# Kernel tuning notes

Measured on AMD Instinct MI355X. Metric: run time of the kernel, lower is better.

Reference implementation:

```python
import jax, jax.numpy as jnp
import numpy as np


def setup_inputs() -> dict:
    key = jax.random.key(0)
    kA, kB = jax.random.split(key)
    B, H, W, C = 1, 80, 80, 256  # NHWC backbone features; B must be 1 for the TF broadcast in the divide to be valid
    feature_A = jax.random.normal(kA, (B, H, W, C), dtype=jnp.float32)
    feature_B = jax.random.normal(kB, (B, H, W, C), dtype=jnp.float32)
    return {"feature_A": feature_A, "feature_B": feature_B}


def reference(feature_A, feature_B):
    # corr[b,i,j,k,l] = mean_c A[b,i,j,c] * B[b,k,l,c]
    # Expressed as a batched matmul instead of materializing the (H,W,H,W,C) intermediate.
    C = feature_A.shape[-1]
    corr = jnp.einsum('bijc,bklc->bijkl', feature_A, feature_B) / C  # [B,H,W,H,W]
    # penalty[b,i,j] = sqrt(sum_{k,l} corr^2)
    penalty = jnp.sqrt(jnp.sum(corr * corr, axis=(-1, -2)))  # [B,H,W]
    # Faithful to tf.math.divide: trailing-dim broadcasting of [B,H,W] against [B,H,W,H,W]
    # (valid because B == 1; penalty aligns to the (j,k,l) trailing axes exactly as in TF).
    return corr / penalty
```

## Files before the change

kernel.cpp:

```cpp
#include <hip/hip_runtime.h>

typedef __attribute__((ext_vector_type(8))) short bf16x8;
typedef __attribute__((ext_vector_type(4))) float f32x4;

#define M_TOT 6400
#define C_TOT 256
#define BM 128
#define BN 128
#define BK 32
#define NTILE 50
#define ONM 50
#define ONN 25

#define VMCNT0 asm volatile("s_waitcnt vmcnt(0)" ::: "memory")
#define VMCNT4 asm volatile("s_waitcnt vmcnt(4)" ::: "memory")
#define VMCNT6 asm volatile("s_waitcnt vmcnt(6)" ::: "memory")
#define SBAR   __builtin_amdgcn_s_barrier()

__device__ __forceinline__ short f2bf(float f) {
    unsigned u = __float_as_uint(f);
    u = (u + 0x7fffu + ((u >> 16) & 1u)) >> 16;
    return (short)u;
}
__device__ __forceinline__ float bf2f(short s) {
    return __uint_as_float(((unsigned)(unsigned short)s) << 16);
}

__device__ __forceinline__ void gload16(const short* g, short* l) {
    __builtin_amdgcn_global_load_lds(
        (const __attribute__((address_space(1))) void*)g,
        (__attribute__((address_space(3))) void*)l, 16, 0, 0);
}


__global__ __launch_bounds__(256) void prep(const float* __restrict__ A,
                                            const float* __restrict__ Bm,
                                            short* __restrict__ Ab,
                                            short* __restrict__ Bb,
                                            short* __restrict__ Bt,
                                            float* __restrict__ P)
{
    __shared__ __align__(16) short Lb[64][72];
    const int bid = blockIdx.x;
    const int t   = threadIdx.x;

    if (bid < 400) {
        const int n0 = (bid % 100) * 64;
        const int c0 = (bid / 100) * 64;
        const int r  = t >> 2;
        const int cb = (t & 3) * 16;

        const float4* src = reinterpret_cast<const float4*>(
            Bm + (size_t)(n0 + r) * C_TOT + c0 + cb);
        const float4 v0 = src[0], v1 = src[1], v2 = src[2], v3 = src[3];
        bf16x8 w0, w1;
        w0[0]=f2bf(v0.x); w0[1]=f2bf(v0.y); w0[2]=f2bf(v0.z); w0[3]=f2bf(v0.w);
        w0[4]=f2bf(v1.x); w0[5]=f2bf(v1.y); w0[6]=f2bf(v1.z); w0[7]=f2bf(v1.w);
        w1[0]=f2bf(v2.x); w1[1]=f2bf(v2.y); w1[2]=f2bf(v2.z); w1[3]=f2bf(v2.w);
        w1[4]=f2bf(v3.x); w1[5]=f2bf(v3.y); w1[6]=f2bf(v3.z); w1[7]=f2bf(v3.w);
        *reinterpret_cast<bf16x8*>(&Lb[r][cb])     = w0;
        *reinterpret_cast<bf16x8*>(&Lb[r][cb + 8]) = w1;
        short* brow = Bb + (size_t)(n0 + r) * C_TOT + c0 + cb;
        *reinterpret_cast<bf16x8*>(brow)     = w0;
        *reinterpret_cast<bf16x8*>(brow + 8) = w1;
        __syncthreads();

        #pragma unroll
        for (int p = 0; p < 2; ++p) {
            const int q = t + p * 256;
            const int c = q >> 3;
            const int h = q & 7;
            bf16x8 w;
            #pragma unroll
            for (int j = 0; j < 8; ++j) w[j] = Lb[h * 8 + j][c];
            *reinterpret_cast<bf16x8*>(&Bt[(size_t)(c0 + c) * M_TOT + n0 + h * 8]) = w;
        }
    } else {
        const int aid = bid - 400;
        if (aid == 0)
            for (int j = t; j < M_TOT; j += 256) P[j] = 0.0f;
        const int base = aid * 2048;
        #pragma unroll
        for (int it = 0; it < 8; ++it) {
            const int i = base + it * 256 + t;
            const float4 v0 = reinterpret_cast<const float4*>(A + (size_t)i * 8)[0];
            const float4 v1 = reinterpret_cast<const float4*>(A + (size_t)i * 8)[1];
            bf16x8 w;
            w[0]=f2bf(v0.x); w[1]=f2bf(v0.y); w[2]=f2bf(v0.z); w[3]=f2bf(v0.w);
            w[4]=f2bf(v1.x); w[5]=f2bf(v1.y); w[6]=f2bf(v1.z); w[7]=f2bf(v1.w);
            *reinterpret_cast<bf16x8*>(Ab + (size_t)i * 8) = w;
        }
    }
}

__global__ __launch_bounds__(256) void convert_ab(const float* __restrict__ A,
                                                  const float* __restrict__ Bm,
                                                  short* __restrict__ Ab,
                                                  short* __restrict__ Bb)
{
    const int n8 = M_TOT * C_TOT / 8;
    for (int i = blockIdx.x * blockDim.x + threadIdx.x; i < 2 * n8;
         i += gridDim.x * blockDim.x) {
        const float* s = (i < n8) ? (A + (size_t)i * 8) : (Bm + (size_t)(i - n8) * 8);
        short* d       = (i < n8) ? (Ab + (size_t)i * 8) : (Bb + (size_t)(i - n8) * 8);
        const float4 v0 = reinterpret_cast<const float4*>(s)[0];
        const float4 v1 = reinterpret_cast<const float4*>(s)[1];
        bf16x8 w;
        w[0]=f2bf(v0.x); w[1]=f2bf(v0.y); w[2]=f2bf(v0.z); w[3]=f2bf(v0.w);
        w[4]=f2bf(v1.x); w[5]=f2bf(v1.y); w[6]=f2bf(v1.z); w[7]=f2bf(v1.w);
        *reinterpret_cast<bf16x8*>(d) = w;
    }
}


__device__ __forceinline__ void stage_tiles_g(const short* __restrict__ A,
                                              const short* __restrict__ B,
                                              int m0, int n0, int k0,
                                              int lda, int ldb,
                                              short* As, short* Bs,
                                              int wave, int lane)
{
    #pragma unroll
    for (int t = 0; t < 2; ++t) {
        const int c  = (wave * 2 + t) * 64 + lane;
        const int r  = c >> 2;
        const int g  = c & 3;
        const int sg = g ^ ((r >> 1) & 3);
        gload16(A + (size_t)(m0 + r) * lda + k0 + sg * 8, As + (wave * 2 + t) * 512);
        gload16(B + (size_t)(n0 + r) * ldb + k0 + sg * 8, Bs + (wave * 2 + t) * 512);
    }
}

template<int KSTEPS>
__device__ __forceinline__ void gemm_tile_g(const short* __restrict__ A,
                                            const short* __restrict__ B,
                                            int m0, int n0, int kbase,
                                            int lda, int ldb, int tid,
                                            short (*Sm)[2][4096],
                                            f32x4 acc[4][4])
{
    const int lane = tid & 63;
    const int wave = tid >> 6;
    const int rl   = lane & 15;
    const int g_rd = lane >> 4;
    const int wr   = wave >> 1;
    const int wc   = wave & 1;

    stage_tiles_g(A, B, m0, n0, kbase, lda, ldb, &Sm[0][0][0], &Sm[0][1][0], wave, lane);
    if (KSTEPS > 1)
        stage_tiles_g(A, B, m0, n0, kbase + BK, lda, ldb,
                      &Sm[1][0][0], &Sm[1][1][0], wave, lane);
    if (KSTEPS > 1) { VMCNT4; } else { VMCNT0; }
    SBAR;

    #pragma unroll
    for (int kt = 0; kt < KSTEPS; ++kt) {
        const int cur = kt % 3;
        if (kt + 2 < KSTEPS)
            stage_tiles_g(A, B, m0, n0, kbase + (kt + 2) * BK, lda, ldb,
                          &Sm[(kt + 2) % 3][0][0], &Sm[(kt + 2) % 3][1][0], wave, lane);

        bf16x8 af[4], bfr[4];
        #pragma unroll
        for (int mi = 0; mi < 4; ++mi) {
            const int r  = wr * 64 + mi * 16 + rl;
            const int sg = g_rd ^ ((r >> 1) & 3);
            af[mi] = *reinterpret_cast<const bf16x8*>(&Sm[cur][0][r * BK + sg * 8]);
        }
        #pragma unroll
        for (int ni = 0; ni < 4; ++ni) {
            const int r  = wc * 64 + ni * 16 + rl;
            const int sg = g_rd ^ ((r >> 1) & 3);
            bfr[ni] = *reinterpret_cast<const bf16x8*>(&Sm[cur][1][r * BK + sg * 8]);
        }
        __builtin_amdgcn_s_setprio(1);
        #pragma unroll
        for (int mi = 0; mi < 4; ++mi)
            #pragma unroll
            for (int ni = 0; ni < 4; ++ni)
                acc[mi][ni] = __builtin_amdgcn_mfma_f32_16x16x32_bf16(
                    af[mi], bfr[ni], acc[mi][ni], 0, 0, 0);
        __builtin_amdgcn_s_setprio(0);

        if (kt + 1 < KSTEPS) {
            if (kt + 2 < KSTEPS) { VMCNT4; } else { VMCNT0; }
            SBAR;
        }
    }
}


template<int STEPS>
__global__ __launch_bounds__(256) void gemm_G(const short* __restrict__ Bt,
                                              float* __restrict__ Gp)
{
    __shared__ __align__(16) short Sm[3][2][4096];
    const int tid = threadIdx.x;
    const int m0 = blockIdx.y * BM, n0 = blockIdx.x * BN;
    const int z  = blockIdx.z;
    f32x4 acc[4][4] = {};
    gemm_tile_g<STEPS>(Bt, Bt, m0, n0, z * (STEPS * BK),
                       M_TOT, M_TOT, tid, Sm, acc);

    float* dst = Gp + (size_t)z * (C_TOT * C_TOT);
    const int lane = tid & 63, rl = lane & 15;
    const int wave = tid >> 6, wr = wave >> 1, wc = wave & 1;
    #pragma unroll
    for (int mi = 0; mi < 4; ++mi)
        #pragma unroll
        for (int i = 0; i < 4; ++i) {
            const int m = m0 + wr * 64 + mi * 16 + (lane >> 4) * 4 + i;
            #pragma unroll
            for (int ni = 0; ni < 4; ++ni)
                dst[m * C_TOT + n0 + wc * 64 + ni * 16 + rl] = acc[mi][ni][i];
        }
}

__global__ __launch_bounds__(256) void g_reduce(const float* __restrict__ Gp,
                                                short* __restrict__ Gb,
                                                int nchunks)
{
    const int i4 = blockIdx.x * 256 + threadIdx.x;
    float4 s = make_float4(0.f, 0.f, 0.f, 0.f);
    for (int z = 0; z < nchunks; ++z) {
        const float4 v = reinterpret_cast<const float4*>(
            Gp + (size_t)z * (C_TOT * C_TOT))[i4];
        s.x += v.x; s.y += v.y; s.z += v.z; s.w += v.w;
    }
    short4 o;
    o.x = f2bf(s.x); o.y = f2bf(s.y); o.z = f2bf(s.z); o.w = f2bf(s.w);
    reinterpret_cast<short4*>(Gb)[i4] = o;
}

__global__ __launch_bounds__(256) void penalty_q(const short* __restrict__ Ab,
                                                 const short* __restrict__ Gb,
                                                 float* __restrict__ P)
{
    __shared__ __align__(16) short Sm[3][2][4096];
    const int tid = threadIdx.x;
    const int m0 = blockIdx.x * BM;
    const int ci = blockIdx.y & 1, cj = blockIdx.y >> 1;
    const int lane = tid & 63, rl = lane & 15;
    const int wave = tid >> 6, wr = wave >> 1, wc = wave & 1;

    f32x4 acc[4][4] = {};
    gemm_tile_g<4>(Ab, Gb + (size_t)(cj * BM) * C_TOT, m0, 0, ci * BM,
                   C_TOT, C_TOT, tid, Sm, acc);

    #pragma unroll
    for (int mi = 0; mi < 4; ++mi)
        #pragma unroll
        for (int i = 0; i < 4; ++i) {
            const int m = m0 + wr * 64 + mi * 16 + (lane >> 4) * 4 + i;
            float s = 0.0f;
            #pragma unroll
            for (int ni = 0; ni < 4; ++ni) {
                const int cp = cj * BM + wc * 64 + ni * 16 + rl;
                s += acc[mi][ni][i] * bf2f(Ab[(size_t)m * C_TOT + cp]);
            }
            s += __shfl_xor(s, 1);
            s += __shfl_xor(s, 2);
            s += __shfl_xor(s, 4);
            s += __shfl_xor(s, 8);
            if (rl == 0) atomicAdd(&P[m], s);
        }
}


#define OBUF 12288
#define OB_B 4096

__device__ __forceinline__ void stage_tiles_o(const short* __restrict__ A,
                                              const short* __restrict__ B,
                                              int m0, int n0, int k0,
                                              short* buf, int wave, int lane)
{
    #pragma unroll
    for (int t = 0; t < 2; ++t) {
        const int c  = (wave * 2 + t) * 64 + lane;
        const int r  = c >> 2;
        const int g  = c & 3;
        const int sg = g ^ ((r >> 1) & 3);
        gload16(A + (size_t)(m0 + r) * C_TOT + k0 + sg * 8, buf + (wave * 2 + t) * 512);
    }
    #pragma unroll
    for (int t = 0; t < 4; ++t) {
        const int c  = (wave * 4 + t) * 64 + lane;
        const int r  = c >> 2;
        const int g  = c & 3;
        const int sg = g ^ ((r >> 1) & 3);
        gload16(B + (size_t)(n0 + r) * C_TOT + k0 + sg * 8,
                buf + OB_B + (wave * 4 + t) * 512);
    }
}

__global__ __launch_bounds__(256, 2) void gemm_out(const short* __restrict__ Ab,
                                                   const short* __restrict__ Bb,
                                                   const float* __restrict__ P,
                                                   float* __restrict__ out)
{
    __shared__ __align__(16) short Sm[3][OBUF];
    const int tid = threadIdx.x;
    const int lane = tid & 63, rl = lane & 15;
    const int g_rd = lane >> 4;
    const int wave = tid >> 6, wr = wave >> 1, wc = wave & 1;

    const int nwg = ONM * ONN, q = nwg >> 3, r = nwg & 7;
    const int orig = blockIdx.x;
    const int xcd = orig & 7, idx = orig >> 3;
    const int wg = (xcd < r ? xcd * (q + 1) : r * (q + 1) + (xcd - r) * q) + idx;
    const int m0 = (wg / ONN) * 128;
    const int n0 = (wg % ONN) * 256;

    f32x4 acc[4][8] = {};

    stage_tiles_o(Ab, Bb, m0, n0, 0,  &Sm[0][0], wave, lane);
    stage_tiles_o(Ab, Bb, m0, n0, BK, &Sm[1][0], wave, lane);
    VMCNT6; SBAR;

    #pragma unroll
    for (int kt = 0; kt < 8; ++kt) {
        const int cur = kt % 3;
        if (kt + 2 < 8)
            stage_tiles_o(Ab, Bb, m0, n0, (kt + 2) * BK, &Sm[(kt + 2) % 3][0], wave, lane);

        bf16x8 af[4], bfr[8];
        #pragma unroll
        for (int mi = 0; mi < 4; ++mi) {
            const int rr = wr * 64 + mi * 16 + rl;
            const int sg = g_rd ^ ((rr >> 1) & 3);
            af[mi] = *reinterpret_cast<const bf16x8*>(&Sm[cur][rr * BK + sg * 8]);
        }
        #pragma unroll
        for (int ni = 0; ni < 8; ++ni) {
            const int rr = wc * 128 + ni * 16 + rl;
            const int sg = g_rd ^ ((rr >> 1) & 3);
            bfr[ni] = *reinterpret_cast<const bf16x8*>(&Sm[cur][OB_B + rr * BK + sg * 8]);
        }
        __builtin_amdgcn_s_setprio(1);
        #pragma unroll
        for (int mi = 0; mi < 4; ++mi)
            #pragma unroll
            for (int ni = 0; ni < 8; ++ni)
                acc[mi][ni] = __builtin_amdgcn_mfma_f32_16x16x32_bf16(
                    af[mi], bfr[ni], acc[mi][ni], 0, 0, 0);
        __builtin_amdgcn_s_setprio(0);

        if (kt + 1 < 8) {
            if (kt + 2 < 8) { VMCNT6; } else { VMCNT0; }
            SBAR;
        }
    }

    float rs[8];
    #pragma unroll
    for (int ni = 0; ni < 8; ++ni)
        rs[ni] = rsqrtf(P[n0 + wc * 128 + ni * 16 + rl]);

    SBAR;

    float* Es = reinterpret_cast<float*>(Sm) + wave * 2112;
    #pragma unroll
    for (int mi = 0; mi < 4; ++mi) {
        #pragma unroll
        for (int ni = 0; ni < 8; ++ni)
            #pragma unroll
            for (int i = 0; i < 4; ++i)
                Es[((lane >> 4) * 4 + i) * 132 + ni * 16 + rl] = acc[mi][ni][i] * rs[ni];
        #pragma unroll
        for (int it = 0; it < 8; ++it) {
            const int f   = it * 64 + lane;
            const int row = f >> 5;
            const int c4  = f & 31;
            const float4 v = *reinterpret_cast<const float4*>(&Es[row * 132 + c4 * 4]);
            const int m = m0 + wr * 64 + mi * 16 + row;
            *reinterpret_cast<float4*>(
                &out[(size_t)m * M_TOT + n0 + wc * 128 + c4 * 4]) = v;
        }
    }
}


__global__ __launch_bounds__(256) void gemm_penalty(const short* __restrict__ Ab,
                                                    const short* __restrict__ Bb,
                                                    float* __restrict__ P)
{
    __shared__ __align__(16) short Sm[3][2][4096];
    const int tid = threadIdx.x;
    const int m0 = blockIdx.y * BM, n0 = blockIdx.x * BN;
    f32x4 acc[4][4] = {};
    gemm_tile_g<8>(Ab, Bb, m0, n0, 0, C_TOT, C_TOT, tid, Sm, acc);

    const int lane = tid & 63, rl = lane & 15;
    const int wave = tid >> 6, wr = wave >> 1;
    #pragma unroll
    for (int mi = 0; mi < 4; ++mi) {
        #pragma unroll
        for (int i = 0; i < 4; ++i) {
            const int m = m0 + wr * 64 + mi * 16 + (lane >> 4) * 4 + i;
            float s = 0.0f;
            #pragma unroll
            for (int ni = 0; ni < 4; ++ni) {
                const float v = acc[mi][ni][i];
                s += v * v;
            }
            s += __shfl_xor(s, 1);
            s += __shfl_xor(s, 2);
            s += __shfl_xor(s, 4);
            s += __shfl_xor(s, 8);
            if (rl == 0) atomicAdd(&P[m], s);
        }
    }
}

__global__ __launch_bounds__(256) void gemm_out_plain(const short* __restrict__ Ab,
                                                      const short* __restrict__ Bb,
                                                      const float* __restrict__ P,
                                                      float* __restrict__ out)
{
    __shared__ __align__(16) short Sm[3][2][4096];
    const int tid = threadIdx.x;
    const int lane = tid & 63, rl = lane & 15;
    const int wave = tid >> 6, wr = wave >> 1, wc = wave & 1;
    const int m0 = blockIdx.y * BM, n0 = blockIdx.x * BN;

    f32x4 acc[4][4] = {};
    gemm_tile_g<8>(Ab, Bb, m0, n0, 0, C_TOT, C_TOT, tid, Sm, acc);

    float rs[4];
    #pragma unroll
    for (int ni = 0; ni < 4; ++ni)
        rs[ni] = rsqrtf(P[n0 + wc * 64 + ni * 16 + rl]);

    SBAR;

    float* Es = reinterpret_cast<float*>(Sm) + wave * 1088;
    #pragma unroll
    for (int mi = 0; mi < 4; ++mi) {
        #pragma unroll
        for (int ni = 0; ni < 4; ++ni)
            #pragma unroll
            for (int i = 0; i < 4; ++i)
                Es[((lane >> 4) * 4 + i) * 68 + ni * 16 + rl] = acc[mi][ni][i] * rs[ni];
        #pragma unroll
        for (int it = 0; it < 4; ++it) {
            const int f   = it * 64 + lane;
            const int row = f >> 4;
            const int c4  = f & 15;
            const float4 v = *reinterpret_cast<const float4*>(&Es[row * 68 + c4 * 4]);
            const int m = m0 + wr * 64 + mi * 16 + row;
            *reinterpret_cast<float4*>(&out[(size_t)m * M_TOT + n0 + wc * 64 + c4 * 4]) = v;
        }
    }
}


__global__ __launch_bounds__(256) void corr_gemm(const float* __restrict__ A,
                                                 const float* __restrict__ Bm,
                                                 float* __restrict__ out,
                                                 float* __restrict__ penalty)
{
    __shared__ short As[BM * BK];
    __shared__ short Bs[BN * BK];

    const int tid  = threadIdx.x;
    const int lane = tid & 63;
    const int wave = tid >> 6;
    const int wr   = wave >> 1;
    const int wc   = wave & 1;
    const int m0   = blockIdx.y * BM;
    const int n0   = blockIdx.x * BN;
    const int g_rd = lane >> 4;
    const int rl   = lane & 15;

    f32x4 acc[4][4] = {};

    for (int k0 = 0; k0 < C_TOT; k0 += BK) {
        #pragma unroll
        for (int half = 0; half < 2; ++half) {
            const int cc = tid + half * 256;
            const int r  = cc >> 2;
            const int g  = cc & 3;
            const int sg = g ^ ((r >> 1) & 3);

            const float4* pa = reinterpret_cast<const float4*>(
                A + (size_t)(m0 + r) * C_TOT + k0 + g * 8);
            float4 a0 = pa[0], a1 = pa[1];
            bf16x8 wa;
            wa[0]=f2bf(a0.x); wa[1]=f2bf(a0.y); wa[2]=f2bf(a0.z); wa[3]=f2bf(a0.w);
            wa[4]=f2bf(a1.x); wa[5]=f2bf(a1.y); wa[6]=f2bf(a1.z); wa[7]=f2bf(a1.w);
            *reinterpret_cast<bf16x8*>(&As[r * BK + sg * 8]) = wa;

            const float4* pb = reinterpret_cast<const float4*>(
                Bm + (size_t)(n0 + r) * C_TOT + k0 + g * 8);
            float4 b0 = pb[0], b1 = pb[1];
            bf16x8 wb;
            wb[0]=f2bf(b0.x); wb[1]=f2bf(b0.y); wb[2]=f2bf(b0.z); wb[3]=f2bf(b0.w);
            wb[4]=f2bf(b1.x); wb[5]=f2bf(b1.y); wb[6]=f2bf(b1.z); wb[7]=f2bf(b1.w);
            *reinterpret_cast<bf16x8*>(&Bs[r * BK + sg * 8]) = wb;
        }
        __syncthreads();

        bf16x8 af[4], bfr[4];
        #pragma unroll
        for (int mi = 0; mi < 4; ++mi) {
            const int r  = wr * 64 + mi * 16 + rl;
            const int sg = g_rd ^ ((r >> 1) & 3);
            af[mi] = *reinterpret_cast<const bf16x8*>(&As[r * BK + sg * 8]);
        }
        #pragma unroll
        for (int ni = 0; ni < 4; ++ni) {
            const int r  = wc * 64 + ni * 16 + rl;
            const int sg = g_rd ^ ((r >> 1) & 3);
            bfr[ni] = *reinterpret_cast<const bf16x8*>(&Bs[r * BK + sg * 8]);
        }
        #pragma unroll
        for (int mi = 0; mi < 4; ++mi)
            #pragma unroll
            for (int ni = 0; ni < 4; ++ni)
                acc[mi][ni] = __builtin_amdgcn_mfma_f32_16x16x32_bf16(
                    af[mi], bfr[ni], acc[mi][ni], 0, 0, 0);
        __syncthreads();
    }

    const float inv_c = 1.0f / (float)C_TOT;
    #pragma unroll
    for (int mi = 0; mi < 4; ++mi) {
        #pragma unroll
        for (int i = 0; i < 4; ++i) {
            const int m = m0 + wr * 64 + mi * 16 + (lane >> 4) * 4 + i;
            float s = 0.0f;
            #pragma unroll
            for (int ni = 0; ni < 4; ++ni) {
                const float v = acc[mi][ni][i] * inv_c;
                out[(size_t)m * M_TOT + n0 + wc * 64 + ni * 16 + rl] = v;
                s += v * v;
            }
            s += __shfl_xor(s, 1);
            s += __shfl_xor(s, 2);
            s += __shfl_xor(s, 4);
            s += __shfl_xor(s, 8);
            if (rl == 0) atomicAdd(&penalty[m], s);
        }
    }
}

__global__ __launch_bounds__(256) void scale_k(float* __restrict__ out,
                                               const float* __restrict__ penalty)
{
    const unsigned cols4 = M_TOT / 4;
    const unsigned total = (unsigned)M_TOT * cols4;
    float4* o4 = reinterpret_cast<float4*>(out);
    const float4* p4 = reinterpret_cast<const float4*>(penalty);
    for (unsigned idx = blockIdx.x * blockDim.x + threadIdx.x; idx < total;
         idx += gridDim.x * blockDim.x) {
        const unsigned n4 = idx % cols4;
        const float4 p = p4[n4];
        float4 v = o4[idx];
        v.x *= rsqrtf(p.x);
        v.y *= rsqrtf(p.y);
        v.z *= rsqrtf(p.z);
        v.w *= rsqrtf(p.w);
        o4[idx] = v;
    }
}


extern "C" void kernel_launch(void* const* d_in, const int* in_sizes, int n_in,
                              void* d_out, int out_size, void* d_ws, size_t ws_size,
                              hipStream_t stream) {
    const float* A = (const float*)d_in[0];
    const float* B = (const float*)d_in[1];
    float* out     = (float*)d_out;

    const size_t mat_sh = (size_t)M_TOT * C_TOT;
    const size_t sz_ab  = mat_sh * sizeof(short);
    const size_t sz_gb  = (size_t)C_TOT * C_TOT * sizeof(short);
    const size_t sz_p   = (size_t)M_TOT * sizeof(float);
    const size_t sz_gq  = (size_t)C_TOT * C_TOT * sizeof(float);
    const size_t base_need = 3 * sz_ab + sz_gb + sz_p;
    const size_t need_f40  = base_need + 40 * sz_gq;
    const size_t need_f20  = base_need + 20 * sz_gq;
    const size_t need_mid  = 2 * sz_ab + sz_p;

    dim3 grid2(NTILE, NTILE);

    if (ws_size >= need_f20) {
        short* Ab = (short*)d_ws;
        short* Bb = Ab + mat_sh;
        short* Bt = Bb + mat_sh;
        short* Gb = Bt + mat_sh;
        float* P  = (float*)((char*)d_ws + 3 * sz_ab + sz_gb);
        float* Gp = (float*)((char*)d_ws + 3 * sz_ab + sz_gb + sz_p);

        prep<<<500, 256, 0, stream>>>(A, B, Ab, Bb, Bt, P);
        if (ws_size >= need_f40) {
            gemm_G<5><<<dim3(2, 2, 40), 256, 0, stream>>>(Bt, Gp);
            g_reduce<<<64, 256, 0, stream>>>(Gp, Gb, 40);
        } else {
            gemm_G<10><<<dim3(2, 2, 20), 256, 0, stream>>>(Bt, Gp);
            g_reduce<<<64, 256, 0, stream>>>(Gp, Gb, 20);
        }
        penalty_q<<<dim3(NTILE, 4), 256, 0, stream>>>(Ab, Gb, P);
        gemm_out<<<ONM * ONN, 256, 0, stream>>>(Ab, Bb, P, out);
    } else if (ws_size >= need_mid) {
        short* Ab = (short*)d_ws;
        short* Bb = Ab + mat_sh;
        float* P  = (float*)(Bb + mat_sh);

        hipMemsetAsync(P, 0, sz_p, stream);
        convert_ab<<<1600, 256, 0, stream>>>(A, B, Ab, Bb);
        gemm_penalty<<<grid2, dim3(256), 0, stream>>>(Ab, Bb, P);
        gemm_out_plain<<<grid2, dim3(256), 0, stream>>>(Ab, Bb, P, out);
    } else {
        float* penalty = (float*)d_ws;
        hipMemsetAsync(penalty, 0, sz_p, stream);
        corr_gemm<<<grid2, dim3(256), 0, stream>>>(A, B, out, penalty);
        scale_k<<<2048, 256, 0, stream>>>(out, penalty);
    }
}
```

Before: 84.01 us.

## Fuse prep, Gram GEMM, reduce and penalty into one cooperative kernel

```diff
diff --git a/kernel.cpp b/kernel.cpp
--- a/kernel.cpp
+++ b/kernel.cpp
@@ -1,4 +1,7 @@
 #include <hip/hip_runtime.h>
+#include <hip/hip_cooperative_groups.h>
+
+namespace cg = cooperative_groups;
 
 typedef __attribute__((ext_vector_type(8))) short bf16x8;
 typedef __attribute__((ext_vector_type(4))) float f32x4;
@@ -11,6 +14,7 @@
 #define NTILE 50
 #define ONM 50
 #define ONN 25
+#define GZ  50
 
 #define VMCNT0 asm volatile("s_waitcnt vmcnt(0)" ::: "memory")
 #define VMCNT4 asm volatile("s_waitcnt vmcnt(4)" ::: "memory")
@@ -30,6 +34,219 @@
     __builtin_amdgcn_global_load_lds(
         (const __attribute__((address_space(1))) void*)g,
         (__attribute__((address_space(3))) void*)l, 16, 0, 0);
+}
+
+
+__device__ __forceinline__ void stage_tiles_g(const short* __restrict__ A,
+                                              const short* __restrict__ B,
+                                              int m0, int n0, int k0,
+                                              int lda, int ldb,
+                                              short* As, short* Bs,
+                                              int wave, int lane)
+{
+    #pragma unroll
+    for (int t = 0; t < 2; ++t) {
+        const int c  = (wave * 2 + t) * 64 + lane;
+        const int r  = c >> 2;
+        const int g  = c & 3;
+        const int sg = g ^ ((r >> 1) & 3);
+        gload16(A + (size_t)(m0 + r) * lda + k0 + sg * 8, As + (wave * 2 + t) * 512);
+        gload16(B + (size_t)(n0 + r) * ldb + k0 + sg * 8, Bs + (wave * 2 + t) * 512);
+    }
+}
+
+template<int KSTEPS>
+__device__ __forceinline__ void gemm_tile_g(const short* __restrict__ A,
+                                            const short* __restrict__ B,
+                                            int m0, int n0, int kbase,
+                                            int lda, int ldb, int tid,
+                                            short (*Sm)[2][4096],
+                                            f32x4 acc[4][4])
+{
+    const int lane = tid & 63;
+    const int wave = tid >> 6;
+    const int rl   = lane & 15;
+    const int g_rd = lane >> 4;
+    const int wr   = wave >> 1;
+    const int wc   = wave & 1;
+
+    stage_tiles_g(A, B, m0, n0, kbase, lda, ldb, &Sm[0][0][0], &Sm[0][1][0], wave, lane);
+    if (KSTEPS > 1)
+        stage_tiles_g(A, B, m0, n0, kbase + BK, lda, ldb,
+                      &Sm[1][0][0], &Sm[1][1][0], wave, lane);
+    if (KSTEPS > 1) { VMCNT4; } else { VMCNT0; }
+    SBAR;
+
+    #pragma unroll
+    for (int kt = 0; kt < KSTEPS; ++kt) {
+        const int cur = kt % 3;
+        if (kt + 2 < KSTEPS)
+            stage_tiles_g(A, B, m0, n0, kbase + (kt + 2) * BK, lda, ldb,
+                          &Sm[(kt + 2) % 3][0][0], &Sm[(kt + 2) % 3][1][0], wave, lane);
+
+        bf16x8 af[4], bfr[4];
+        #pragma unroll
+        for (int mi = 0; mi < 4; ++mi) {
+            const int r  = wr * 64 + mi * 16 + rl;
+            const int sg = g_rd ^ ((r >> 1) & 3);
+            af[mi] = *reinterpret_cast<const bf16x8*>(&Sm[cur][0][r * BK + sg * 8]);
+        }
+        #pragma unroll
+        for (int ni = 0; ni < 4; ++ni) {
+            const int r  = wc * 64 + ni * 16 + rl;
+            const int sg = g_rd ^ ((r >> 1) & 3);
+            bfr[ni] = *reinterpret_cast<const bf16x8*>(&Sm[cur][1][r * BK + sg * 8]);
+        }
+        __builtin_amdgcn_s_setprio(1);
+        #pragma unroll
+        for (int mi = 0; mi < 4; ++mi)
+            #pragma unroll
+            for (int ni = 0; ni < 4; ++ni)
+                acc[mi][ni] = __builtin_amdgcn_mfma_f32_16x16x32_bf16(
+                    af[mi], bfr[ni], acc[mi][ni], 0, 0, 0);
+        __builtin_amdgcn_s_setprio(0);
+
+        if (kt + 1 < KSTEPS) {
+            if (kt + 2 < KSTEPS) { VMCNT4; } else { VMCNT0; }
+            SBAR;
+        }
+    }
+}
+
+
+__global__ __launch_bounds__(256) void fused_pre(const float* __restrict__ A,
+                                                 const float* __restrict__ Bm,
+                                                 short* __restrict__ Ab,
+                                                 short* __restrict__ Bb,
+                                                 short* __restrict__ Bt,
+                                                 short* __restrict__ Gb,
+                                                 float* __restrict__ P,
+                                                 float* __restrict__ Gp)
+{
+    cg::grid_group grid = cg::this_grid();
+    __shared__ __align__(16) short Sm[3][2][4096];
+    const int bid = blockIdx.x;
+    const int t   = threadIdx.x;
+
+    for (int u = bid; u < 500; u += 256) {
+        if (u < 400) {
+            short (*Lb)[72] = reinterpret_cast<short(*)[72]>(&Sm[0][0][0]);
+            const int n0 = (u % 100) * 64;
+            const int c0 = (u / 100) * 64;
+            const int r  = t >> 2;
+            const int cb = (t & 3) * 16;
+
+            const float4* src = reinterpret_cast<const float4*>(
+                Bm + (size_t)(n0 + r) * C_TOT + c0 + cb);
+            const float4 v0 = src[0], v1 = src[1], v2 = src[2], v3 = src[3];
+            bf16x8 w0, w1;
+            w0[0]=f2bf(v0.x); w0[1]=f2bf(v0.y); w0[2]=f2bf(v0.z); w0[3]=f2bf(v0.w);
+            w0[4]=f2bf(v1.x); w0[5]=f2bf(v1.y); w0[6]=f2bf(v1.z); w0[7]=f2bf(v1.w);
+            w1[0]=f2bf(v2.x); w1[1]=f2bf(v2.y); w1[2]=f2bf(v2.z); w1[3]=f2bf(v2.w);
+            w1[4]=f2bf(v3.x); w1[5]=f2bf(v3.y); w1[6]=f2bf(v3.z); w1[7]=f2bf(v3.w);
+            *reinterpret_cast<bf16x8*>(&Lb[r][cb])     = w0;
+            *reinterpret_cast<bf16x8*>(&Lb[r][cb + 8]) = w1;
+            short* brow = Bb + (size_t)(n0 + r) * C_TOT + c0 + cb;
+            *reinterpret_cast<bf16x8*>(brow)     = w0;
+            *reinterpret_cast<bf16x8*>(brow + 8) = w1;
+            __syncthreads();
+
+            #pragma unroll
+            for (int p = 0; p < 2; ++p) {
+                const int q = t + p * 256;
+                const int c = q >> 3;
+                const int h = q & 7;
+                bf16x8 w;
+                #pragma unroll
+                for (int j = 0; j < 8; ++j) w[j] = Lb[h * 8 + j][c];
+                *reinterpret_cast<bf16x8*>(&Bt[(size_t)(c0 + c) * M_TOT + n0 + h * 8]) = w;
+            }
+            __syncthreads();
+        } else {
+            const int aid = u - 400;
+            if (aid == 0)
+                for (int j = t; j < M_TOT; j += 256) P[j] = 0.0f;
+            const int base = aid * 2048;
+            #pragma unroll
+            for (int it = 0; it < 8; ++it) {
+                const int i = base + it * 256 + t;
+                const float4 v0 = reinterpret_cast<const float4*>(A + (size_t)i * 8)[0];
+                const float4 v1 = reinterpret_cast<const float4*>(A + (size_t)i * 8)[1];
+                bf16x8 w;
+                w[0]=f2bf(v0.x); w[1]=f2bf(v0.y); w[2]=f2bf(v0.z); w[3]=f2bf(v0.w);
+                w[4]=f2bf(v1.x); w[5]=f2bf(v1.y); w[6]=f2bf(v1.z); w[7]=f2bf(v1.w);
+                *reinterpret_cast<bf16x8*>(Ab + (size_t)i * 8) = w;
+            }
+        }
+    }
+    grid.sync();
+
+    if (bid < 4 * GZ) {
+        const int z  = bid >> 2;
+        const int qd = bid & 3;
+        const int m0 = (qd & 1) * BM, n0 = (qd >> 1) * BN;
+        f32x4 acc[4][4] = {};
+        gemm_tile_g<4>(Bt, Bt, m0, n0, z * 128, M_TOT, M_TOT, t, Sm, acc);
+
+        float* dst = Gp + (size_t)z * (C_TOT * C_TOT);
+        const int lane = t & 63, rl = lane & 15;
+        const int wave = t >> 6, wr = wave >> 1, wc = wave & 1;
+        #pragma unroll
+        for (int mi = 0; mi < 4; ++mi)
+            #pragma unroll
+            for (int i = 0; i < 4; ++i) {
+                const int m = m0 + wr * 64 + mi * 16 + (lane >> 4) * 4 + i;
+                #pragma unroll
+                for (int ni = 0; ni < 4; ++ni)
+                    dst[m * C_TOT + n0 + wc * 64 + ni * 16 + rl] = acc[mi][ni][i];
+            }
+    }
+    grid.sync();
+
+    if (bid < 64) {
+        const int i4 = bid * 256 + t;
+        float4 s = make_float4(0.f, 0.f, 0.f, 0.f);
+        for (int z = 0; z < GZ; ++z) {
+            const float4 v = reinterpret_cast<const float4*>(
+                Gp + (size_t)z * (C_TOT * C_TOT))[i4];
+            s.x += v.x; s.y += v.y; s.z += v.z; s.w += v.w;
+        }
+        short4 o;
+        o.x = f2bf(s.x); o.y = f2bf(s.y); o.z = f2bf(s.z); o.w = f2bf(s.w);
+        reinterpret_cast<short4*>(Gb)[i4] = o;
+    }
+    grid.sync();
+
+    if (bid < 200) {
+        const int mt = bid % 50;
+        const int qd = bid / 50;
+        const int ci = qd & 1, cj = qd >> 1;
+        const int m0 = mt * BM;
+        const int lane = t & 63, rl = lane & 15;
+        const int wave = t >> 6, wr = wave >> 1, wc = wave & 1;
+
+        f32x4 acc[4][4] = {};
+        gemm_tile_g<4>(Ab, Gb + (size_t)(cj * BM) * C_TOT, m0, 0, ci * BM,
+                       C_TOT, C_TOT, t, Sm, acc);
+
+        #pragma unroll
+        for (int mi = 0; mi < 4; ++mi)
+            #pragma unroll
+            for (int i = 0; i < 4; ++i) {
+                const int m = m0 + wr * 64 + mi * 16 + (lane >> 4) * 4 + i;
+                float s = 0.0f;
+                #pragma unroll
+                for (int ni = 0; ni < 4; ++ni) {
+                    const int cp = cj * BM + wc * 64 + ni * 16 + rl;
+                    s += acc[mi][ni][i] * bf2f(Ab[(size_t)m * C_TOT + cp]);
+                }
+                s += __shfl_xor(s, 1);
+                s += __shfl_xor(s, 2);
+                s += __shfl_xor(s, 4);
+                s += __shfl_xor(s, 8);
+                if (rl == 0) atomicAdd(&P[m], s);
+            }
+    }
 }
 
 
@@ -93,6 +310,197 @@
     }
 }
 
+template<int STEPS>
+__global__ __launch_bounds__(256) void gemm_G(const short* __restrict__ Bt,
+                                              float* __restrict__ Gp)
+{
+    __shared__ __align__(16) short Sm[3][2][4096];
+    const int tid = threadIdx.x;
+    const int m0 = blockIdx.y * BM, n0 = blockIdx.x * BN;
+    const int z  = blockIdx.z;
+    f32x4 acc[4][4] = {};
+    gemm_tile_g<STEPS>(Bt, Bt, m0, n0, z * (STEPS * BK),
+                       M_TOT, M_TOT, tid, Sm, acc);
+
+    float* dst = Gp + (size_t)z * (C_TOT * C_TOT);
+    const int lane = tid & 63, rl = lane & 15;
+    const int wave = tid >> 6, wr = wave >> 1, wc = wave & 1;
+    #pragma unroll
+    for (int mi = 0; mi < 4; ++mi)
+        #pragma unroll
+        for (int i = 0; i < 4; ++i) {
+            const int m = m0 + wr * 64 + mi * 16 + (lane >> 4) * 4 + i;
+            #pragma unroll
+            for (int ni = 0; ni < 4; ++ni)
+                dst[m * C_TOT + n0 + wc * 64 + ni * 16 + rl] = acc[mi][ni][i];
+        }
+}
+
+__global__ __launch_bounds__(256) void g_reduce(const float* __restrict__ Gp,
+                                                short* __restrict__ Gb,
+                                                int nchunks)
+{
+    const int i4 = blockIdx.x * 256 + threadIdx.x;
+    float4 s = make_float4(0.f, 0.f, 0.f, 0.f);
+    for (int z = 0; z < nchunks; ++z) {
+        const float4 v = reinterpret_cast<const float4*>(
+            Gp + (size_t)z * (C_TOT * C_TOT))[i4];
+        s.x += v.x; s.y += v.y; s.z += v.z; s.w += v.w;
+    }
+    short4 o;
+    o.x = f2bf(s.x); o.y = f2bf(s.y); o.z = f2bf(s.z); o.w = f2bf(s.w);
+    reinterpret_cast<short4*>(Gb)[i4] = o;
+}
+
+__global__ __launch_bounds__(256) void penalty_q(const short* __restrict__ Ab,
+                                                 const short* __restrict__ Gb,
+                                                 float* __restrict__ P)
+{
+    __shared__ __align__(16) short Sm[3][2][4096];
+    const int tid = threadIdx.x;
+    const int m0 = blockIdx.x * BM;
+    const int ci = blockIdx.y & 1, cj = blockIdx.y >> 1;
+    const int lane = tid & 63, rl = lane & 15;
+    const int wave = tid >> 6, wr = wave >> 1, wc = wave & 1;
+
+    f32x4 acc[4][4] = {};
+    gemm_tile_g<4>(Ab, Gb + (size_t)(cj * BM) * C_TOT, m0, 0, ci * BM,
+                   C_TOT, C_TOT, tid, Sm, acc);
+
+    #pragma unroll
+    for (int mi = 0; mi < 4; ++mi)
+        #pragma unroll
+        for (int i = 0; i < 4; ++i) {
+            const int m = m0 + wr * 64 + mi * 16 + (lane >> 4) * 4 + i;
+            float s = 0.0f;
+            #pragma unroll
+            for (int ni = 0; ni < 4; ++ni) {
+                const int cp = cj * BM + wc * 64 + ni * 16 + rl;
+                s += acc[mi][ni][i] * bf2f(Ab[(size_t)m * C_TOT + cp]);
+            }
+            s += __shfl_xor(s, 1);
+            s += __shfl_xor(s, 2);
+            s += __shfl_xor(s, 4);
+            s += __shfl_xor(s, 8);
+            if (rl == 0) atomicAdd(&P[m], s);
+        }
+}
+
+
+#define OBUF 12288
+#define OB_B 4096
+
+__device__ __forceinline__ void stage_tiles_o(const short* __restrict__ A,
+                                              const short* __restrict__ B,
+                                              int m0, int n0, int k0,
+                                              short* buf, int wave, int lane)
+{
+    #pragma unroll
+    for (int t = 0; t < 2; ++t) {
+        const int c  = (wave * 2 + t) * 64 + lane;
+        const int r  = c >> 2;
+        const int g  = c & 3;
+        const int sg = g ^ ((r >> 1) & 3);
+        gload16(A + (size_t)(m0 + r) * C_TOT + k0 + sg * 8, buf + (wave * 2 + t) * 512);
+    }
+    #pragma unroll
+    for (int t = 0; t < 4; ++t) {
+        const int c  = (wave * 4 + t) * 64 + lane;
+        const int r  = c >> 2;
+        const int g  = c & 3;
+        const int sg = g ^ ((r >> 1) & 3);
+        gload16(B + (size_t)(n0 + r) * C_TOT + k0 + sg * 8,
+                buf + OB_B + (wave * 4 + t) * 512);
+    }
+}
+
+__global__ __launch_bounds__(256, 2) void gemm_out(const short* __restrict__ Ab,
+                                                   const short* __restrict__ Bb,
+                                                   const float* __restrict__ P,
+                                                   float* __restrict__ out)
+{
+    __shared__ __align__(16) short Sm[3][OBUF];
+    const int tid = threadIdx.x;
+    const int lane = tid & 63, rl = lane & 15;
+    const int g_rd = lane >> 4;
+    const int wave = tid >> 6, wr = wave >> 1, wc = wave & 1;
+
+    const int nwg = ONM * ONN, q = nwg >> 3, r = nwg & 7;
+    const int orig = blockIdx.x;
+    const int xcd = orig & 7, idx = orig >> 3;
+    const int wg = (xcd < r ? xcd * (q + 1) : r * (q + 1) + (xcd - r) * q) + idx;
+    const int m0 = (wg / ONN) * 128;
+    const int n0 = (wg % ONN) * 256;
+
+    f32x4 acc[4][8] = {};
+
+    stage_tiles_o(Ab, Bb, m0, n0, 0,  &Sm[0][0], wave, lane);
+    stage_tiles_o(Ab, Bb, m0, n0, BK, &Sm[1][0], wave, lane);
+    VMCNT6; SBAR;
+
+    #pragma unroll
+    for (int kt = 0; kt < 8; ++kt) {
+        const int cur = kt % 3;
+        if (kt + 2 < 8)
+            stage_tiles_o(Ab, Bb, m0, n0, (kt + 2) * BK, &Sm[(kt + 2) % 3][0], wave, lane);
+
+        bf16x8 af[4], bfr[8];
+        #pragma unroll
+        for (int mi = 0; mi < 4; ++mi) {
+            const int rr = wr * 64 + mi * 16 + rl;
+            const int sg = g_rd ^ ((rr >> 1) & 3);
+            af[mi] = *reinterpret_cast<const bf16x8*>(&Sm[cur][rr * BK + sg * 8]);
+        }
+        #pragma unroll
+        for (int ni = 0; ni < 8; ++ni) {
+            const int rr = wc * 128 + ni * 16 + rl;
+            const int sg = g_rd ^ ((rr >> 1) & 3);
+            bfr[ni] = *reinterpret_cast<const bf16x8*>(&Sm[cur][OB_B + rr * BK + sg * 8]);
+        }
+        __builtin_amdgcn_s_setprio(1);
+        #pragma unroll
+        for (int mi = 0; mi < 4; ++mi)
+            #pragma unroll
+            for (int ni = 0; ni < 8; ++ni)
+                acc[mi][ni] = __builtin_amdgcn_mfma_f32_16x16x32_bf16(
+                    af[mi], bfr[ni], acc[mi][ni], 0, 0, 0);
+        __builtin_amdgcn_s_setprio(0);
+
+        if (kt + 1 < 8) {
+            if (kt + 2 < 8) { VMCNT6; } else { VMCNT0; }
+            SBAR;
+        }
+    }
+
+    float rs[8];
+    #pragma unroll
+    for (int ni = 0; ni < 8; ++ni)
+        rs[ni] = rsqrtf(P[n0 + wc * 128 + ni * 16 + rl]);
+
+    SBAR;
+
+    float* Es = reinterpret_cast<float*>(Sm) + wave * 2112;
+    #pragma unroll
+    for (int mi = 0; mi < 4; ++mi) {
+        #pragma unroll
+        for (int ni = 0; ni < 8; ++ni)
+            #pragma unroll
+            for (int i = 0; i < 4; ++i)
+                Es[((lane >> 4) * 4 + i) * 132 + ni * 16 + rl] = acc[mi][ni][i] * rs[ni];
+        #pragma unroll
+        for (int it = 0; it < 8; ++it) {
+            const int f   = it * 64 + lane;
+            const int row = f >> 5;
+            const int c4  = f & 31;
+            const f32x4 v = *reinterpret_cast<const f32x4*>(&Es[row * 132 + c4 * 4]);
+            const int m = m0 + wr * 64 + mi * 16 + row;
+            __builtin_nontemporal_store(v, reinterpret_cast<f32x4*>(
+                &out[(size_t)m * M_TOT + n0 + wc * 128 + c4 * 4]));
+        }
+    }
+}
+
+
 __global__ __launch_bounds__(256) void convert_ab(const float* __restrict__ A,
                                                   const float* __restrict__ Bm,
                                                   short* __restrict__ Ab,
@@ -111,275 +519,6 @@
         *reinterpret_cast<bf16x8*>(d) = w;
     }
 }
-
-
-__device__ __forceinline__ void stage_tiles_g(const short* __restrict__ A,
-                                              const short* __restrict__ B,
-                                              int m0, int n0, int k0,
-                                              int lda, int ldb,
-                                              short* As, short* Bs,
-                                              int wave, int lane)
-{
-    #pragma unroll
-    for (int t = 0; t < 2; ++t) {
-        const int c  = (wave * 2 + t) * 64 + lane;
-        const int r  = c >> 2;
-        const int g  = c & 3;
-        const int sg = g ^ ((r >> 1) & 3);
-        gload16(A + (size_t)(m0 + r) * lda + k0 + sg * 8, As + (wave * 2 + t) * 512);
-        gload16(B + (size_t)(n0 + r) * ldb + k0 + sg * 8, Bs + (wave * 2 + t) * 512);
-    }
-}
-
-template<int KSTEPS>
-__device__ __forceinline__ void gemm_tile_g(const short* __restrict__ A,
-                                            const short* __restrict__ B,
-                                            int m0, int n0, int kbase,
-                                            int lda, int ldb, int tid,
-                                            short (*Sm)[2][4096],
-                                            f32x4 acc[4][4])
-{
-    const int lane = tid & 63;
-    const int wave = tid >> 6;
-    const int rl   = lane & 15;
-    const int g_rd = lane >> 4;
-    const int wr   = wave >> 1;
-    const int wc   = wave & 1;
-
-    stage_tiles_g(A, B, m0, n0, kbase, lda, ldb, &Sm[0][0][0], &Sm[0][1][0], wave, lane);
-    if (KSTEPS > 1)
-        stage_tiles_g(A, B, m0, n0, kbase + BK, lda, ldb,
-                      &Sm[1][0][0], &Sm[1][1][0], wave, lane);
-    if (KSTEPS > 1) { VMCNT4; } else { VMCNT0; }
-    SBAR;
-
-    #pragma unroll
-    for (int kt = 0; kt < KSTEPS; ++kt) {
-        const int cur = kt % 3;
-        if (kt + 2 < KSTEPS)
-            stage_tiles_g(A, B, m0, n0, kbase + (kt + 2) * BK, lda, ldb,
-                          &Sm[(kt + 2) % 3][0][0], &Sm[(kt + 2) % 3][1][0], wave, lane);
-
-        bf16x8 af[4], bfr[4];
-        #pragma unroll
-        for (int mi = 0; mi < 4; ++mi) {
-            const int r  = wr * 64 + mi * 16 + rl;
-            const int sg = g_rd ^ ((r >> 1) & 3);
-            af[mi] = *reinterpret_cast<const bf16x8*>(&Sm[cur][0][r * BK + sg * 8]);
-        }
-        #pragma unroll
-        for (int ni = 0; ni < 4; ++ni) {
-            const int r  = wc * 64 + ni * 16 + rl;
-            const int sg = g_rd ^ ((r >> 1) & 3);
-            bfr[ni] = *reinterpret_cast<const bf16x8*>(&Sm[cur][1][r * BK + sg * 8]);
-        }
-        __builtin_amdgcn_s_setprio(1);
-        #pragma unroll
-        for (int mi = 0; mi < 4; ++mi)
-            #pragma unroll
-            for (int ni = 0; ni < 4; ++ni)
-                acc[mi][ni] = __builtin_amdgcn_mfma_f32_16x16x32_bf16(
-                    af[mi], bfr[ni], acc[mi][ni], 0, 0, 0);
-        __builtin_amdgcn_s_setprio(0);
-
-        if (kt + 1 < KSTEPS) {
-            if (kt + 2 < KSTEPS) { VMCNT4; } else { VMCNT0; }
-            SBAR;
-        }
-    }
-}
-
-
-template<int STEPS>
-__global__ __launch_bounds__(256) void gemm_G(const short* __restrict__ Bt,
-                                              float* __restrict__ Gp)
-{
-    __shared__ __align__(16) short Sm[3][2][4096];
-    const int tid = threadIdx.x;
-    const int m0 = blockIdx.y * BM, n0 = blockIdx.x * BN;
-    const int z  = blockIdx.z;
-    f32x4 acc[4][4] = {};
-    gemm_tile_g<STEPS>(Bt, Bt, m0, n0, z * (STEPS * BK),
-                       M_TOT, M_TOT, tid, Sm, acc);
-
-    float* dst = Gp + (size_t)z * (C_TOT * C_TOT);
-    const int lane = tid & 63, rl = lane & 15;
-    const int wave = tid >> 6, wr = wave >> 1, wc = wave & 1;
-    #pragma unroll
-    for (int mi = 0; mi < 4; ++mi)
-        #pragma unroll
-        for (int i = 0; i < 4; ++i) {
-            const int m = m0 + wr * 64 + mi * 16 + (lane >> 4) * 4 + i;
-            #pragma unroll
-            for (int ni = 0; ni < 4; ++ni)
-                dst[m * C_TOT + n0 + wc * 64 + ni * 16 + rl] = acc[mi][ni][i];
-        }
-}
-
-__global__ __launch_bounds__(256) void g_reduce(const float* __restrict__ Gp,
-                                                short* __restrict__ Gb,
-                                                int nchunks)
-{
-    const int i4 = blockIdx.x * 256 + threadIdx.x;
-    float4 s = make_float4(0.f, 0.f, 0.f, 0.f);
-    for (int z = 0; z < nchunks; ++z) {
-        const float4 v = reinterpret_cast<const float4*>(
-            Gp + (size_t)z * (C_TOT * C_TOT))[i4];
-        s.x += v.x; s.y += v.y; s.z += v.z; s.w += v.w;
-    }
-    short4 o;
-    o.x = f2bf(s.x); o.y = f2bf(s.y); o.z = f2bf(s.z); o.w = f2bf(s.w);
-    reinterpret_cast<short4*>(Gb)[i4] = o;
-}
-
-__global__ __launch_bounds__(256) void penalty_q(const short* __restrict__ Ab,
-                                                 const short* __restrict__ Gb,
-                                                 float* __restrict__ P)
-{
-    __shared__ __align__(16) short Sm[3][2][4096];
-    const int tid = threadIdx.x;
-    const int m0 = blockIdx.x * BM;
-    const int ci = blockIdx.y & 1, cj = blockIdx.y >> 1;
-    const int lane = tid & 63, rl = lane & 15;
-    const int wave = tid >> 6, wr = wave >> 1, wc = wave & 1;
-
-    f32x4 acc[4][4] = {};
-    gemm_tile_g<4>(Ab, Gb + (size_t)(cj * BM) * C_TOT, m0, 0, ci * BM,
-                   C_TOT, C_TOT, tid, Sm, acc);
-
-    #pragma unroll
-    for (int mi = 0; mi < 4; ++mi)
-        #pragma unroll
-        for (int i = 0; i < 4; ++i) {
-            const int m = m0 + wr * 64 + mi * 16 + (lane >> 4) * 4 + i;
-            float s = 0.0f;
-            #pragma unroll
-            for (int ni = 0; ni < 4; ++ni) {
-                const int cp = cj * BM + wc * 64 + ni * 16 + rl;
-                s += acc[mi][ni][i] * bf2f(Ab[(size_t)m * C_TOT + cp]);
-            }
-            s += __shfl_xor(s, 1);
-            s += __shfl_xor(s, 2);
-            s += __shfl_xor(s, 4);
-            s += __shfl_xor(s, 8);
-            if (rl == 0) atomicAdd(&P[m], s);
-        }
-}
-
-
-#define OBUF 12288
-#define OB_B 4096
-
-__device__ __forceinline__ void stage_tiles_o(const short* __restrict__ A,
-                                              const short* __restrict__ B,
-                                              int m0, int n0, int k0,
-                                              short* buf, int wave, int lane)
-{
-    #pragma unroll
-    for (int t = 0; t < 2; ++t) {
-        const int c  = (wave * 2 + t) * 64 + lane;
-        const int r  = c >> 2;
-        const int g  = c & 3;
-        const int sg = g ^ ((r >> 1) & 3);
-        gload16(A + (size_t)(m0 + r) * C_TOT + k0 + sg * 8, buf + (wave * 2 + t) * 512);
-    }
-    #pragma unroll
-    for (int t = 0; t < 4; ++t) {
-        const int c  = (wave * 4 + t) * 64 + lane;
-        const int r  = c >> 2;
-        const int g  = c & 3;
-        const int sg = g ^ ((r >> 1) & 3);
-        gload16(B + (size_t)(n0 + r) * C_TOT + k0 + sg * 8,
-                buf + OB_B + (wave * 4 + t) * 512);
-    }
-}
-
-__global__ __launch_bounds__(256, 2) void gemm_out(const short* __restrict__ Ab,
-                                                   const short* __restrict__ Bb,
-                                                   const float* __restrict__ P,
-                                                   float* __restrict__ out)
-{
-    __shared__ __align__(16) short Sm[3][OBUF];
-    const int tid = threadIdx.x;
-    const int lane = tid & 63, rl = lane & 15;
-    const int g_rd = lane >> 4;
-    const int wave = tid >> 6, wr = wave >> 1, wc = wave & 1;
-
-    const int nwg = ONM * ONN, q = nwg >> 3, r = nwg & 7;
-    const int orig = blockIdx.x;
-    const int xcd = orig & 7, idx = orig >> 3;
-    const int wg = (xcd < r ? xcd * (q + 1) : r * (q + 1) + (xcd - r) * q) + idx;
-    const int m0 = (wg / ONN) * 128;
-    const int n0 = (wg % ONN) * 256;
-
-    f32x4 acc[4][8] = {};
-
-    stage_tiles_o(Ab, Bb, m0, n0, 0,  &Sm[0][0], wave, lane);
-    stage_tiles_o(Ab, Bb, m0, n0, BK, &Sm[1][0], wave, lane);
-    VMCNT6; SBAR;
-
-    #pragma unroll
-    for (int kt = 0; kt < 8; ++kt) {
-        const int cur = kt % 3;
-        if (kt + 2 < 8)
-            stage_tiles_o(Ab, Bb, m0, n0, (kt + 2) * BK, &Sm[(kt + 2) % 3][0], wave, lane);
-
-        bf16x8 af[4], bfr[8];
-        #pragma unroll
-        for (int mi = 0; mi < 4; ++mi) {
-            const int rr = wr * 64 + mi * 16 + rl;
-            const int sg = g_rd ^ ((rr >> 1) & 3);
-            af[mi] = *reinterpret_cast<const bf16x8*>(&Sm[cur][rr * BK + sg * 8]);
-        }
-        #pragma unroll
-        for (int ni = 0; ni < 8; ++ni) {
-            const int rr = wc * 128 + ni * 16 + rl;
-            const int sg = g_rd ^ ((rr >> 1) & 3);
-            bfr[ni] = *reinterpret_cast<const bf16x8*>(&Sm[cur][OB_B + rr * BK + sg * 8]);
-        }
-        __builtin_amdgcn_s_setprio(1);
-        #pragma unroll
-        for (int mi = 0; mi < 4; ++mi)
-            #pragma unroll
-            for (int ni = 0; ni < 8; ++ni)
-                acc[mi][ni] = __builtin_amdgcn_mfma_f32_16x16x32_bf16(
-                    af[mi], bfr[ni], acc[mi][ni], 0, 0, 0);
-        __builtin_amdgcn_s_setprio(0);
-
-        if (kt + 1 < 8) {
-            if (kt + 2 < 8) { VMCNT6; } else { VMCNT0; }
-            SBAR;
-        }
-    }
-
-    float rs[8];
-    #pragma unroll
-    for (int ni = 0; ni < 8; ++ni)
-        rs[ni] = rsqrtf(P[n0 + wc * 128 + ni * 16 + rl]);
-
-    SBAR;
-
-    float* Es = reinterpret_cast<float*>(Sm) + wave * 2112;
-    #pragma unroll
-    for (int mi = 0; mi < 4; ++mi) {
-        #pragma unroll
-        for (int ni = 0; ni < 8; ++ni)
-            #pragma unroll
-            for (int i = 0; i < 4; ++i)
-                Es[((lane >> 4) * 4 + i) * 132 + ni * 16 + rl] = acc[mi][ni][i] * rs[ni];
-        #pragma unroll
-        for (int it = 0; it < 8; ++it) {
-            const int f   = it * 64 + lane;
-            const int row = f >> 5;
-            const int c4  = f & 31;
-            const float4 v = *reinterpret_cast<const float4*>(&Es[row * 132 + c4 * 4]);
-            const int m = m0 + wr * 64 + mi * 16 + row;
-            *reinterpret_cast<float4*>(
-                &out[(size_t)m * M_TOT + n0 + wc * 128 + c4 * 4]) = v;
-        }
-    }
-}
-
 
 __global__ __launch_bounds__(256) void gemm_penalty(const short* __restrict__ Ab,
                                                     const short* __restrict__ Bb,
@@ -579,13 +718,36 @@
     const size_t sz_p   = (size_t)M_TOT * sizeof(float);
     const size_t sz_gq  = (size_t)C_TOT * C_TOT * sizeof(float);
     const size_t base_need = 3 * sz_ab + sz_gb + sz_p;
+    const size_t need_f50  = base_need + (size_t)GZ * sz_gq;
     const size_t need_f40  = base_need + 40 * sz_gq;
     const size_t need_f20  = base_need + 20 * sz_gq;
     const size_t need_mid  = 2 * sz_ab + sz_p;
 
     dim3 grid2(NTILE, NTILE);
 
-    if (ws_size >= need_f20) {
+    int coop = 0;
+    {
+        int dev = 0;
+        (void)hipGetDevice(&dev);
+        (void)hipDeviceGetAttribute(&coop, hipDeviceAttributeCooperativeLaunch, dev);
+    }
+
+    if (ws_size >= need_f50 && coop) {
+        const float* Aa = A;
+        const float* Ba = B;
+        short* Ab = (short*)d_ws;
+        short* Bb = Ab + mat_sh;
+        short* Bt = Bb + mat_sh;
+        short* Gb = Bt + mat_sh;
+        float* P  = (float*)((char*)d_ws + 3 * sz_ab + sz_gb);
+        float* Gp = (float*)((char*)d_ws + 3 * sz_ab + sz_gb + sz_p);
+
+        void* args[] = { (void*)&Aa, (void*)&Ba, (void*)&Ab, (void*)&Bb,
+                         (void*)&Bt, (void*)&Gb, (void*)&P, (void*)&Gp };
+        (void)hipLaunchCooperativeKernel((const void*)fused_pre, dim3(256), dim3(256),
+                                         args, 0, stream);
+        gemm_out<<<ONM * ONN, 256, 0, stream>>>(Ab, Bb, P, out);
+    } else if (ws_size >= need_f20) {
         short* Ab = (short*)d_ws;
         short* Bb = Ab + mat_sh;
         short* Bt = Bb + mat_sh;
@@ -608,13 +770,13 @@
         short* Bb = Ab + mat_sh;
         float* P  = (float*)(Bb + mat_sh);
 
-        hipMemsetAsync(P, 0, sz_p, stream);
+        (void)hipMemsetAsync(P, 0, sz_p, stream);
         convert_ab<<<1600, 256, 0, stream>>>(A, B, Ab, Bb);
         gemm_penalty<<<grid2, dim3(256), 0, stream>>>(Ab, Bb, P);
         gemm_out_plain<<<grid2, dim3(256), 0, stream>>>(Ab, Bb, P, out);
     } else {
         float* penalty = (float*)d_ws;
-        hipMemsetAsync(penalty, 0, sz_p, stream);
+        (void)hipMemsetAsync(penalty, 0, sz_p, stream);
         corr_gemm<<<grid2, dim3(256), 0, stream>>>(A, B, out, penalty);
         scale_k<<<2048, 256, 0, stream>>>(out, penalty);
     }
```

Measured after the change: 179.8 us. 114% more time.
